# Performance work log

Measured on AMD Instinct MI355X. Metric: run time of the kernel, lower is better.

The kernel has to match this reference:

```python
import jax, jax.numpy as jnp
import numpy as np

D_MODEL = 2048
N_HEADS = 16
HEAD_DIM = D_MODEL // N_HEADS
ROPE_BASE = 10000.0
B, T = 2, 2048


def setup_inputs() -> dict:
    key = jax.random.key(0)
    k1, k2, k3 = jax.random.split(key, 3)
    s_in = 1.0 / np.sqrt(D_MODEL)
    x = jax.random.normal(k1, (B, T, D_MODEL), dtype=jnp.float32)
    Wqkv = jax.random.normal(k2, (3 * D_MODEL, D_MODEL), dtype=jnp.float32) * s_in
    bqkv = jnp.zeros((3 * D_MODEL,), dtype=jnp.float32)
    Wo = jax.random.normal(k3, (D_MODEL, D_MODEL), dtype=jnp.float32) * s_in
    bo = jnp.zeros((D_MODEL,), dtype=jnp.float32)
    return {"x": x, "Wqkv": Wqkv, "bqkv": bqkv, "Wo": Wo, "bo": bo}


def _rotate_half(x):
    # [x1,x2,x3,x4] -> [-x2,x1,-x4,x3] (interleaved pairs)
    x_even = x[..., 0::2]
    x_odd = x[..., 1::2]
    return jnp.stack((-x_odd, x_even), axis=-1).reshape(x.shape)


def _rope_cos_sin(seq_len, dtype):
    half = HEAD_DIM // 2
    inv_freq = 1.0 / (ROPE_BASE ** (jnp.arange(half, dtype=jnp.float32) / half))
    freqs = jnp.arange(seq_len, dtype=jnp.float32)[:, None] * inv_freq[None, :]  # (T, half)
    emb = jnp.repeat(freqs, 2, axis=-1)  # (T, D) interleaved
    cos = jnp.cos(emb).astype(dtype)[None, None]  # (1,1,T,D)
    sin = jnp.sin(emb).astype(dtype)[None, None]
    return cos, sin


def reference(x, Wqkv, bqkv, Wo, bo):
    b, t, c = x.shape
    qkv = jnp.einsum('btc,fc->btf', x, Wqkv) + bqkv  # (B,T,3C)
    q, k, v = jnp.split(qkv, 3, axis=-1)
    def to_heads(z):
        return z.reshape(b, t, N_HEADS, HEAD_DIM).transpose(0, 2, 1, 3)  # (B,H,T,D)
    q, k, v = to_heads(q), to_heads(k), to_heads(v)
    cos, sin = _rope_cos_sin(t, x.dtype)
    q = q * cos + _rotate_half(q) * sin
    k = k * cos + _rotate_half(k) * sin
    scale = 1.0 / jnp.sqrt(jnp.asarray(HEAD_DIM, dtype=x.dtype))
    scores = jnp.einsum('bhqd,bhkd->bhqk', q, k) * scale  # (B,H,T,T)
    causal = jnp.tril(jnp.ones((t, t), dtype=bool))
    scores = jnp.where(causal, scores, jnp.finfo(scores.dtype).min)
    attn = jax.nn.softmax(scores, axis=-1)
    out = jnp.einsum('bhqk,bhkd->bhqd', attn, v)  # (B,H,T,D)
    out = out.transpose(0, 2, 1, 3).reshape(b, t, c)
    return jnp.einsum('btc,oc->bto', out, Wo) + bo
```

## Files before the change

kernel.cpp:

```cpp
#include <hip/hip_runtime.h>

using f16 = _Float16;
typedef _Float16 h8 __attribute__((ext_vector_type(8)));
typedef _Float16 h4 __attribute__((ext_vector_type(4)));
typedef float f4 __attribute__((ext_vector_type(4)));
typedef unsigned int u32;
typedef unsigned long long u64;

#define DEVI static __device__ __forceinline__

DEVI f4 mfma16(h8 a, h8 b, f4 c) {
  return __builtin_amdgcn_mfma_f32_16x16x32_f16(a, b, c, 0, 0, 0);
}

DEVI void gl_lds16(const f16* g, f16* l) {
  __builtin_amdgcn_global_load_lds(
      (const __attribute__((address_space(1))) u32*)g,
      (__attribute__((address_space(3))) u32*)l, 16, 0, 0);
}

DEVI u32 pkh2(float a, float b) {
  union { f16 h[2]; u32 u; } x;
  x.h[0] = (f16)a; x.h[1] = (f16)b;
  return x.u;
}

typedef float fv4 __attribute__((ext_vector_type(4)));

__global__ __launch_bounds__(256) void k_cvt(const float* __restrict__ in,
                                             f16* __restrict__ out, int n4) {
  int i = blockIdx.x * 256 + threadIdx.x;
  if (i >= n4) return;
  fv4 v = ((const fv4*)in)[i];
  h4 o;
  o[0] = (f16)v[0]; o[1] = (f16)v[1]; o[2] = (f16)v[2]; o[3] = (f16)v[3];
  ((h4*)out)[i] = o;
}

__global__ __launch_bounds__(256) void k_rope_tbl(float* __restrict__ tbl) {
  int i = blockIdx.x * 256 + threadIdx.x;
  int t = i >> 6, d = i & 63;
  float invf = exp2f(-(float)d * (13.287712379549449f / 64.f));
  float a = (float)t * invf;
  tbl[2 * i]     = cosf(a);
  tbl[2 * i + 1] = sinf(a);
}

template <int F32OUT>
__global__ __launch_bounds__(512, 2) void k_gemm256(const f16* __restrict__ A,
                                                    const f16* __restrict__ Bt,
                                                    const float* __restrict__ bias,
                                                    void* __restrict__ Cp,
                                                    int M, int N, int K, int gy) {
  __shared__ f16 lds[2][32768];
  const int tid = threadIdx.x;
  const int w = tid >> 6, lane = tid & 63;
  const int g = lane >> 4, colq = lane & 15;
  const int wr = w >> 2, wc = w & 3;
  const int sw = (colq >> 1) & 3;
  const int rdc = (g ^ sw) << 3;

  const int nwg = gridDim.x;
  const int q8 = nwg >> 3;
  const int swz = (blockIdx.x & 7) * q8 + (blockIdx.x >> 3);
  const int bm = swz % gy, bn = swz / gy;

  const f16* Ab = A + (size_t)bm * 256 * K;
  const f16* Bb = Bt + (size_t)bn * 256 * K;
  const int nt = K >> 6;

  const int srow = lane >> 2;
  const int schunk = (lane & 3) ^ ((lane >> 3) & 3);

  auto STAGE_A = [&](int kt, int h, f16* buf) {
    const int k0 = (kt << 6) + (h << 5);
#pragma unroll
    for (int j = 0; j < 2; ++j) {
      const int r = (w * 2 + j) * 16;
      gl_lds16(Ab + (size_t)(r + srow) * K + k0 + schunk * 8, buf + h * 8192 + r * 32);
    }
  };
  auto STAGE_B = [&](int kt, int h, f16* buf) {
    const int k0 = (kt << 6) + (h << 5);
#pragma unroll
    for (int j = 0; j < 2; ++j) {
      const int r = (w * 2 + j) * 16;
      gl_lds16(Bb + (size_t)(r + srow) * K + k0 + schunk * 8, buf + 16384 + h * 8192 + r * 32);
    }
  };

  f4 acc[8][4] = {};

  auto LDA = [&](h8* dst, int mh, int h, const f16* cur) {
#pragma unroll
    for (int m = 0; m < 4; ++m) {
      const int row = wr * 128 + (mh * 4 + m) * 16 + colq;
      dst[m] = *(const h8*)(cur + h * 8192 + row * 32 + rdc);
    }
  };
  auto LDB = [&](h8* dst, int h, const f16* cur) {
#pragma unroll
    for (int n = 0; n < 4; ++n) {
      const int row = wc * 64 + n * 16 + colq;
      dst[n] = *(const h8*)(cur + 16384 + h * 8192 + row * 32 + rdc);
    }
  };
  auto MM = [&](h8* af, h8* bf, int mh) {
#pragma unroll
    for (int m = 0; m < 4; ++m)
#pragma unroll
      for (int n = 0; n < 4; ++n)
        acc[mh * 4 + m][n] = mfma16(af[m], bf[n], acc[mh * 4 + m][n]);
  };

  STAGE_A(0, 0, lds[0]); STAGE_B(0, 0, lds[0]);
  STAGE_A(0, 1, lds[0]); STAGE_B(0, 1, lds[0]);
  STAGE_A(1, 0, lds[1]); STAGE_B(1, 0, lds[1]);
  asm volatile("s_waitcnt vmcnt(4)" ::: "memory");
  __builtin_amdgcn_s_barrier();

  for (int t = 0; t < nt; ++t) {
    f16* cur = lds[t & 1];
    f16* nxt = lds[(t & 1) ^ 1];
    const bool m1 = (t + 1 < nt), m2 = (t + 2 < nt);
    h8 af[4], bf[4];
    LDA(af, 0, 0, cur);
    LDB(bf, 0, cur);
    if (m1) STAGE_A(t + 1, 1, nxt);
    __builtin_amdgcn_s_barrier();
    __builtin_amdgcn_s_setprio(1);
    MM(af, bf, 0);
    __builtin_amdgcn_s_setprio(0);
    __builtin_amdgcn_s_barrier();
    LDA(af, 1, 0, cur);
    if (m1) STAGE_B(t + 1, 1, nxt);
    __builtin_amdgcn_s_barrier();
    __builtin_amdgcn_s_setprio(1);
    MM(af, bf, 1);
    __builtin_amdgcn_s_setprio(0);
    __builtin_amdgcn_s_barrier();
    LDA(af, 0, 1, cur);
    LDB(bf, 1, cur);
    if (m2) STAGE_A(t + 2, 0, cur);
    __builtin_amdgcn_s_barrier();
    __builtin_amdgcn_s_setprio(1);
    MM(af, bf, 0);
    __builtin_amdgcn_s_setprio(0);
    __builtin_amdgcn_s_barrier();
    LDA(af, 1, 1, cur);
    if (m2) STAGE_B(t + 2, 0, cur);
    __builtin_amdgcn_s_barrier();
    __builtin_amdgcn_s_setprio(1);
    MM(af, bf, 1);
    __builtin_amdgcn_s_setprio(0);
    if (m2) {
      asm volatile("s_waitcnt vmcnt(4)" ::: "memory");
    } else {
      asm volatile("s_waitcnt vmcnt(0)" ::: "memory");
    }
    __builtin_amdgcn_s_barrier();
  }

#pragma unroll
  for (int n = 0; n < 4; ++n) {
    const int col = bn * 256 + wc * 64 + n * 16 + colq;
    const float bv = bias[col];
#pragma unroll
    for (int m = 0; m < 8; ++m) {
      const int row0 = bm * 256 + wr * 128 + m * 16 + 4 * g;
#pragma unroll
      for (int r = 0; r < 4; ++r) {
        float v = acc[m][n][r] + bv;
        if constexpr (F32OUT) {
          ((float*)Cp)[(size_t)(row0 + r) * N + col] = v;
        } else {
          ((f16*)Cp)[(size_t)(row0 + r) * N + col] = (f16)v;
        }
      }
    }
  }
}

template <int F32OUT>
__global__ __launch_bounds__(512, 2) void k_gemm128(const f16* __restrict__ A,
                                                    const f16* __restrict__ Bt,
                                                    const float* __restrict__ bias,
                                                    void* __restrict__ Cp,
                                                    int M, int N, int K, int gy) {
  __shared__ f16 lds[2][24576];
  const int tid = threadIdx.x;
  const int w = tid >> 6, lane = tid & 63;
  const int g = lane >> 4, colq = lane & 15;
  const int wr = w >> 2, wc = w & 3;

  const int nwg = gridDim.x;
  const int q8 = nwg >> 3;
  const int swz = (blockIdx.x & 7) * q8 + (blockIdx.x >> 3);
  const int bm = swz % gy, bn = swz / gy;

  const f16* Ab = A + (size_t)bm * 128 * K;
  const f16* Bb = Bt + (size_t)bn * 256 * K;

  const int srow = lane >> 3;
  const int schunk = (lane & 7) ^ srow;
  const int nt = K >> 6;

  auto STAGE = [&](int kt, f16* buf) {
    const int k0 = kt << 6;
    f16* bA = buf;
    f16* bB = buf + 128 * 64;
#pragma unroll
    for (int j = 0; j < 2; ++j) {
      const int r = w * 16 + j * 8;
      gl_lds16(Ab + (size_t)(r + srow) * K + k0 + schunk * 8, bA + r * 64);
    }
#pragma unroll
    for (int j = 0; j < 4; ++j) {
      const int r = w * 32 + j * 8;
      gl_lds16(Bb + (size_t)(r + srow) * K + k0 + schunk * 8, bB + r * 64);
    }
  };

  STAGE(0, lds[0]);
  STAGE(1, lds[1]);
  asm volatile("s_waitcnt vmcnt(6)" ::: "memory");
  __builtin_amdgcn_s_barrier();

  f4 acc[4][4] = {};
  const int rowA0 = wr * 64 + colq;
  const int rowB0 = wc * 64 + colq;
  const int cq7 = colq & 7;

  for (int t = 0; t < nt; ++t) {
    f16* cur = lds[t & 1];
    h8 af[2][4], bf[2][4];
#pragma unroll
    for (int kki = 0; kki < 2; ++kki) {
#pragma unroll
      for (int m = 0; m < 4; ++m)
        af[kki][m] = *(const h8*)(cur + (rowA0 + m * 16) * 64 + (((kki * 4 + g) ^ cq7) * 8));
#pragma unroll
      for (int n = 0; n < 4; ++n)
        bf[kki][n] = *(const h8*)(cur + 8192 + (rowB0 + n * 16) * 64 + (((kki * 4 + g) ^ cq7) * 8));
    }
    asm volatile("s_waitcnt lgkmcnt(0)" ::: "memory");
    __builtin_amdgcn_s_barrier();
    const bool more = (t + 2 < nt);
    if (more) STAGE(t + 2, cur);
    __builtin_amdgcn_s_setprio(1);
#pragma unroll
    for (int m = 0; m < 4; ++m)
#pragma unroll
      for (int n = 0; n < 4; ++n)
#pragma unroll
        for (int kki = 0; kki < 2; ++kki)
          acc[m][n] = mfma16(af[kki][m], bf[kki][n], acc[m][n]);
    __builtin_amdgcn_s_setprio(0);
    if (more) {
      asm volatile("s_waitcnt vmcnt(6)" ::: "memory");
    } else {
      asm volatile("s_waitcnt vmcnt(0)" ::: "memory");
    }
    __builtin_amdgcn_s_barrier();
  }

#pragma unroll
  for (int n = 0; n < 4; ++n) {
    const int col = bn * 256 + wc * 64 + n * 16 + colq;
    const float bv = bias[col];
#pragma unroll
    for (int m = 0; m < 4; ++m) {
      const int row0 = bm * 128 + wr * 64 + m * 16 + 4 * g;
#pragma unroll
      for (int r = 0; r < 4; ++r) {
        float v = acc[m][n][r] + bv;
        if constexpr (F32OUT) {
          ((float*)Cp)[(size_t)(row0 + r) * N + col] = v;
        } else {
          ((f16*)Cp)[(size_t)(row0 + r) * N + col] = (f16)v;
        }
      }
    }
  }
}

__global__ __launch_bounds__(256) void k_rope(const f16* __restrict__ qkv,
                                              const float* __restrict__ tbl,
                                              f16* __restrict__ Q, f16* __restrict__ K) {
  int i = blockIdx.x * 256 + threadIdx.x;
  int d = i & 63;
  int h = (i >> 6) & 15;
  int bt = i >> 10;
  int t = bt & 2047;
  int bh = ((bt >> 11) << 4) | h;
  union { u32 u; f16 h2[2]; } qa, ka, qo, ko;
  qa.u = *(const u32*)(qkv + (size_t)bt * 6144 + h * 128 + 2 * d);
  ka.u = *(const u32*)(qkv + (size_t)bt * 6144 + 2048 + h * 128 + 2 * d);
  float c = tbl[2 * (t * 64 + d)];
  float s = tbl[2 * (t * 64 + d) + 1];
  float q0f = (float)qa.h2[0], q1f = (float)qa.h2[1];
  float k0f = (float)ka.h2[0], k1f = (float)ka.h2[1];
  const float SQ = 0.088388347648318447f * 1.4426950408889634f;
  qo.h2[0] = (f16)((q0f * c - q1f * s) * SQ);
  qo.h2[1] = (f16)((q1f * c + q0f * s) * SQ);
  ko.h2[0] = (f16)(k0f * c - k1f * s);
  ko.h2[1] = (f16)(k1f * c + k0f * s);
  *(u32*)(Q + ((size_t)bh * 2048 + t) * 128 + 2 * d) = qo.u;
  *(u32*)(K + ((size_t)bh * 2048 + t) * 128 + 2 * d) = ko.u;
}

__global__ __launch_bounds__(256) void k_vtrans(const f16* __restrict__ qkv,
                                                f16* __restrict__ Vt) {
  __shared__ f16 ldsT[128 * 40];
  const int bh = blockIdx.y, t0 = blockIdx.x * 32;
  const int b = bh >> 4, h = bh & 15;
  const int tid = threadIdx.x;
#pragma unroll
  for (int cc = 0; cc < 2; ++cc) {
    int task = tid + cc * 256;
    int row = task >> 4;
    int ch = task & 15;
    h8 v = *(const h8*)(qkv + (size_t)(b * 2048 + t0 + row) * 6144 + 4096 + h * 128 + ch * 8);
#pragma unroll
    for (int j = 0; j < 8; ++j) ldsT[(ch * 8 + j) * 40 + row] = v[j];
  }
  __syncthreads();
  int d = tid >> 1, seg = tid & 1;
  h8 v0 = *(const h8*)(ldsT + d * 40 + seg * 16);
  h8 v1 = *(const h8*)(ldsT + d * 40 + seg * 16 + 8);
  f16* dst = Vt + ((size_t)bh * 128 + d) * 2048 + t0 + seg * 16;
  *(h8*)dst = v0;
  *(h8*)(dst + 8) = v1;
}

DEVI void stage_tiles(const f16* __restrict__ Kg, const f16* __restrict__ Vtg,
                      f16* bufK, f16* bufV, int kv, int w, int lane) {
#pragma unroll
  for (int jj = 0; jj < 4; ++jj) {
    const int j = w * 4 + jj;
    const int rK = j * 4 + (lane >> 4);
    const int cK = (lane & 15) ^ ((rK & 7) << 1);
    gl_lds16(Kg + (size_t)(kv + rK) * 128 + cK * 8, bufK + j * 512);
    const int rV = j * 8 + (lane >> 3);
    const int cV = (lane & 7) ^ (rV & 7);
    gl_lds16(Vtg + (size_t)rV * 2048 + kv + cV * 8, bufV + j * 512);
  }
}

__global__ __launch_bounds__(256, 1) void k_attn(const f16* __restrict__ Q,
                                                 const f16* __restrict__ K,
                                                 const f16* __restrict__ Vt,
                                                 f16* __restrict__ O) {
  __shared__ f16 lds[2][16384];
  const int tid = threadIdx.x;
  const int w = tid >> 6, lane = tid & 63;
  const int g = lane >> 4, q = lane & 15;
  const int bid = blockIdx.x;
  const int bh = bid & 31;
  const int b = bid >> 5;

  const f16* Kg = K + (size_t)bh * 2048 * 128;
  const f16* Vtg = Vt + (size_t)bh * 128 * 2048;
  const int qx2 = (q & 7) << 1;
  const int qx = q & 7;

  for (int ph = 0; ph < 2; ++ph) {
    const int p = ph ? (15 - b) : b;
    const int q0w = p * 128 + w * 32;
    const int nit = 2 * (p + 1);

    h8 qf[2][4];
#pragma unroll
    for (int set = 0; set < 2; ++set)
#pragma unroll
      for (int d4 = 0; d4 < 4; ++d4)
        qf[set][d4] = *(const h8*)(Q + ((size_t)bh * 2048 + q0w + 16 * set + q) * 128 + d4 * 32 + g * 8);

    stage_tiles(Kg, Vtg, lds[0], lds[0] + 8192, 0, w, lane);
    asm volatile("s_waitcnt vmcnt(0)" ::: "memory");
    __builtin_amdgcn_s_barrier();

    f4 ot[2][8] = {};
    float mrun[2] = {-3.0e38f, -3.0e38f};
    float lrun[2] = {0.f, 0.f};

    for (int it = 0; it < nit; ++it) {
      const int kv0 = it * 64;
      f16* bufK = lds[it & 1];
      f16* bufV = bufK + 8192;
      if (it + 1 < nit) {
        f16* nb = lds[(it + 1) & 1];
        stage_tiles(Kg, Vtg, nb, nb + 8192, kv0 + 64, w, lane);
      }
      if (kv0 < q0w + 32) {
        f4 st[2][4] = {{{0.f,0.f,0.f,0.f},{0.f,0.f,0.f,0.f},{0.f,0.f,0.f,0.f},{0.f,0.f,0.f,0.f}},
                       {{0.f,0.f,0.f,0.f},{0.f,0.f,0.f,0.f},{0.f,0.f,0.f,0.f},{0.f,0.f,0.f,0.f}}};
#pragma unroll
        for (int d4 = 0; d4 < 4; ++d4) {
          h8 kf[4];
#pragma unroll
          for (int s = 0; s < 4; ++s)
            kf[s] = *(const h8*)(bufK + ((16 * s + q) * 16 + ((4 * d4 + g) ^ qx2)) * 8);
#pragma unroll
          for (int set = 0; set < 2; ++set)
#pragma unroll
            for (int s = 0; s < 4; ++s)
              st[set][s] = mfma16(kf[s], qf[set][d4], st[set][s]);
        }
        if (kv0 + 63 > q0w) {
#pragma unroll
          for (int set = 0; set < 2; ++set) {
            const int qcol = q0w + 16 * set + q;
#pragma unroll
            for (int s = 0; s < 4; ++s)
#pragma unroll
              for (int r = 0; r < 4; ++r)
                if (kv0 + s * 16 + 4 * g + r > qcol) st[set][s][r] = -3.0e38f;
          }
        }
        float pm[2];
#pragma unroll
        for (int set = 0; set < 2; ++set) {
          float m0 = st[set][0][0];
#pragma unroll
          for (int s = 0; s < 4; ++s)
#pragma unroll
            for (int r = 0; r < 4; ++r) m0 = fmaxf(m0, st[set][s][r]);
          m0 = fmaxf(m0, __shfl_xor(m0, 16));
          m0 = fmaxf(m0, __shfl_xor(m0, 32));
          pm[set] = m0;
        }
        const bool ok = (pm[0] <= mrun[0] + 8.0f) && (pm[1] <= mrun[1] + 8.0f);
        if (!__all(ok)) {
#pragma unroll
          for (int set = 0; set < 2; ++set) {
            float mnew = fmaxf(mrun[set], pm[set]);
            float corr = exp2f(mrun[set] - mnew);
            lrun[set] *= corr;
#pragma unroll
            for (int dt = 0; dt < 8; ++dt) ot[set][dt] *= corr;
            mrun[set] = mnew;
          }
        }
#pragma unroll
        for (int set = 0; set < 2; ++set) {
          float ps = 0.f;
#pragma unroll
          for (int s = 0; s < 4; ++s)
#pragma unroll
            for (int r = 0; r < 4; ++r) {
              st[set][s][r] = exp2f(st[set][s][r] - mrun[set]);
              ps += st[set][s][r];
            }
          ps += __shfl_xor(ps, 16);
          ps += __shfl_xor(ps, 32);
          lrun[set] += ps;
        }
        union { u32 u[4]; h8 h; } pb[2][2];
        const int s0l = ((g & 1) << 5) | q;
        const bool hi = g >= 2;
#pragma unroll
        for (int set = 0; set < 2; ++set)
#pragma unroll
          for (int hh = 0; hh < 2; ++hh) {
            u32 wA0 = pkh2(st[set][2 * hh][0], st[set][2 * hh][1]);
            u32 wB0 = pkh2(st[set][2 * hh][2], st[set][2 * hh][3]);
            u32 wA1 = pkh2(st[set][2 * hh + 1][0], st[set][2 * hh + 1][1]);
            u32 wB1 = pkh2(st[set][2 * hh + 1][2], st[set][2 * hh + 1][3]);
            u32 a0 = (u32)__shfl((int)wA0, s0l),      a1 = (u32)__shfl((int)wA1, s0l);
            u32 b0 = (u32)__shfl((int)wB0, s0l),      b1 = (u32)__shfl((int)wB1, s0l);
            u32 c0 = (u32)__shfl((int)wA0, s0l + 16), c1 = (u32)__shfl((int)wA1, s0l + 16);
            u32 d0 = (u32)__shfl((int)wB0, s0l + 16), d1 = (u32)__shfl((int)wB1, s0l + 16);
            pb[set][hh].u[0] = hi ? a1 : a0;
            pb[set][hh].u[1] = hi ? b1 : b0;
            pb[set][hh].u[2] = hi ? c1 : c0;
            pb[set][hh].u[3] = hi ? d1 : d0;
          }
#pragma unroll
        for (int hh = 0; hh < 2; ++hh)
#pragma unroll
          for (int dt = 0; dt < 8; ++dt) {
            h8 vf = *(const h8*)(bufV + ((dt * 16 + q) * 8 + ((4 * hh + g) ^ qx)) * 8);
#pragma unroll
            for (int set = 0; set < 2; ++set)
              ot[set][dt] = mfma16(vf, pb[set][hh].h, ot[set][dt]);
          }
      }
      asm volatile("s_waitcnt vmcnt(0)" ::: "memory");
      __builtin_amdgcn_s_barrier();
    }

#pragma unroll
    for (int set = 0; set < 2; ++set) {
      float linv = 1.0f / lrun[set];
      f16* Ob = O + ((size_t)(bh >> 4) * 2048 + q0w + 16 * set + q) * 2048 + (bh & 15) * 128 + 4 * g;
#pragma unroll
      for (int dt = 0; dt < 8; ++dt) {
        union { f16 hh4[4]; u64 u; } o;
#pragma unroll
        for (int r = 0; r < 4; ++r) o.hh4[r] = (f16)(ot[set][dt][r] * linv);
        *(u64*)(Ob + dt * 16) = o.u;
      }
    }
  }
}

extern "C" void kernel_launch(void* const* d_in, const int* in_sizes, int n_in,
                              void* d_out, int out_size, void* d_ws, size_t ws_size,
                              hipStream_t stream) {
  (void)in_sizes; (void)n_in; (void)out_size; (void)ws_size;
  const float* x    = (const float*)d_in[0];
  const float* Wqkv = (const float*)d_in[1];
  const float* bqkv = (const float*)d_in[2];
  const float* Wo   = (const float*)d_in[3];
  const float* bo   = (const float*)d_in[4];

  char* ws = (char*)d_ws;
  f16* xb    = (f16*)ws; ws += (size_t)4096 * 2048 * 2;
  f16* wqkvb = (f16*)ws; ws += (size_t)6144 * 2048 * 2;
  f16* wob   = (f16*)ws; ws += (size_t)2048 * 2048 * 2;
  f16* qkvb  = (f16*)ws; ws += (size_t)4096 * 6144 * 2;
  f16* Qb    = (f16*)ws; ws += (size_t)32 * 2048 * 128 * 2;
  f16* Kb    = (f16*)ws; ws += (size_t)32 * 2048 * 128 * 2;
  f16* Vtb   = (f16*)ws; ws += (size_t)32 * 128 * 2048 * 2;
  f16* attb  = (f16*)ws; ws += (size_t)4096 * 2048 * 2;
  float* tbl = (float*)ws; ws += (size_t)2048 * 64 * 2 * 4;

  k_cvt<<<8192, 256, 0, stream>>>(x, xb, 2097152);
  k_cvt<<<12288, 256, 0, stream>>>(Wqkv, wqkvb, 3145728);
  k_cvt<<<4096, 256, 0, stream>>>(Wo, wob, 1048576);
  k_rope_tbl<<<512, 256, 0, stream>>>(tbl);

  k_gemm256<0><<<384, 512, 0, stream>>>(xb, wqkvb, bqkv, qkvb, 4096, 6144, 2048, 16);

  k_rope<<<16384, 256, 0, stream>>>(qkvb, tbl, Qb, Kb);
  k_vtrans<<<dim3(64, 32), 256, 0, stream>>>(qkvb, Vtb);

  k_attn<<<256, 256, 0, stream>>>(Qb, Kb, Vtb, attb);

  k_gemm128<1><<<256, 512, 0, stream>>>(attb, wob, bo, d_out, 4096, 2048, 2048, 32);
}
```

Before: 326.2 us.

## Double-buffer GEMM register fragments and fuse RoPE with V transpose kernel

The QKV GEMM main loop now keeps two sets of A/B fragments, so the LDS reads for the next MFMA quarter are issued before the current MFMAs, and half of the barriers are removed. Launch bounds drop from two to one workgroup per CU to make room for the extra registers. Separately, the RoPE kernel is merged into the V-transpose kernel, which removes one launch and lets the Q/K rotation share a pass over each tile. Removing barriers risks LDS races with the staging writes, and the lower occupancy could reduce latency hiding.

```diff
diff --git a/kernel.cpp b/kernel.cpp
--- a/kernel.cpp
+++ b/kernel.cpp
@@ -47,7 +47,7 @@
 }
 
 template <int F32OUT>
-__global__ __launch_bounds__(512, 2) void k_gemm256(const f16* __restrict__ A,
+__global__ __launch_bounds__(512, 1) void k_gemm256(const f16* __restrict__ A,
                                                     const f16* __restrict__ Bt,
                                                     const float* __restrict__ bias,
                                                     void* __restrict__ Cp,
@@ -119,39 +119,36 @@
   asm volatile("s_waitcnt vmcnt(4)" ::: "memory");
   __builtin_amdgcn_s_barrier();
 
+  h8 af0[4], af1[4], bf0[4], bf1[4];
+
   for (int t = 0; t < nt; ++t) {
     f16* cur = lds[t & 1];
     f16* nxt = lds[(t & 1) ^ 1];
     const bool m1 = (t + 1 < nt), m2 = (t + 2 < nt);
-    h8 af[4], bf[4];
-    LDA(af, 0, 0, cur);
-    LDB(bf, 0, cur);
+    LDA(af0, 0, 0, cur);
+    LDB(bf0, 0, cur);
     if (m1) STAGE_A(t + 1, 1, nxt);
-    __builtin_amdgcn_s_barrier();
+    LDA(af1, 1, 0, cur);
     __builtin_amdgcn_s_setprio(1);
-    MM(af, bf, 0);
+    MM(af0, bf0, 0);
     __builtin_amdgcn_s_setprio(0);
     __builtin_amdgcn_s_barrier();
-    LDA(af, 1, 0, cur);
     if (m1) STAGE_B(t + 1, 1, nxt);
-    __builtin_amdgcn_s_barrier();
+    LDA(af0, 0, 1, cur);
+    LDB(bf1, 1, cur);
     __builtin_amdgcn_s_setprio(1);
-    MM(af, bf, 1);
+    MM(af1, bf0, 1);
     __builtin_amdgcn_s_setprio(0);
     __builtin_amdgcn_s_barrier();
-    LDA(af, 0, 1, cur);
-    LDB(bf, 1, cur);
     if (m2) STAGE_A(t + 2, 0, cur);
-    __builtin_amdgcn_s_barrier();
+    LDA(af1, 1, 1, cur);
     __builtin_amdgcn_s_setprio(1);
-    MM(af, bf, 0);
+    MM(af0, bf1, 0);
     __builtin_amdgcn_s_setprio(0);
     __builtin_amdgcn_s_barrier();
-    LDA(af, 1, 1, cur);
     if (m2) STAGE_B(t + 2, 0, cur);
-    __builtin_amdgcn_s_barrier();
     __builtin_amdgcn_s_setprio(1);
-    MM(af, bf, 1);
+    MM(af1, bf1, 1);
     __builtin_amdgcn_s_setprio(0);
     if (m2) {
       asm volatile("s_waitcnt vmcnt(4)" ::: "memory");
@@ -284,33 +281,10 @@
   }
 }
 
-__global__ __launch_bounds__(256) void k_rope(const f16* __restrict__ qkv,
-                                              const float* __restrict__ tbl,
-                                              f16* __restrict__ Q, f16* __restrict__ K) {
-  int i = blockIdx.x * 256 + threadIdx.x;
-  int d = i & 63;
-  int h = (i >> 6) & 15;
-  int bt = i >> 10;
-  int t = bt & 2047;
-  int bh = ((bt >> 11) << 4) | h;
-  union { u32 u; f16 h2[2]; } qa, ka, qo, ko;
-  qa.u = *(const u32*)(qkv + (size_t)bt * 6144 + h * 128 + 2 * d);
-  ka.u = *(const u32*)(qkv + (size_t)bt * 6144 + 2048 + h * 128 + 2 * d);
-  float c = tbl[2 * (t * 64 + d)];
-  float s = tbl[2 * (t * 64 + d) + 1];
-  float q0f = (float)qa.h2[0], q1f = (float)qa.h2[1];
-  float k0f = (float)ka.h2[0], k1f = (float)ka.h2[1];
-  const float SQ = 0.088388347648318447f * 1.4426950408889634f;
-  qo.h2[0] = (f16)((q0f * c - q1f * s) * SQ);
-  qo.h2[1] = (f16)((q1f * c + q0f * s) * SQ);
-  ko.h2[0] = (f16)(k0f * c - k1f * s);
-  ko.h2[1] = (f16)(k1f * c + k0f * s);
-  *(u32*)(Q + ((size_t)bh * 2048 + t) * 128 + 2 * d) = qo.u;
-  *(u32*)(K + ((size_t)bh * 2048 + t) * 128 + 2 * d) = ko.u;
-}
-
-__global__ __launch_bounds__(256) void k_vtrans(const f16* __restrict__ qkv,
-                                                f16* __restrict__ Vt) {
+__global__ __launch_bounds__(256) void k_ropev(const f16* __restrict__ qkv,
+                                               const float* __restrict__ tbl,
+                                               f16* __restrict__ Q, f16* __restrict__ K,
+                                               f16* __restrict__ Vt) {
   __shared__ f16 ldsT[128 * 40];
   const int bh = blockIdx.y, t0 = blockIdx.x * 32;
   const int b = bh >> 4, h = bh & 15;
@@ -323,6 +297,28 @@
     h8 v = *(const h8*)(qkv + (size_t)(b * 2048 + t0 + row) * 6144 + 4096 + h * 128 + ch * 8);
 #pragma unroll
     for (int j = 0; j < 8; ++j) ldsT[(ch * 8 + j) * 40 + row] = v[j];
+  }
+  const float SQ = 0.088388347648318447f * 1.4426950408889634f;
+#pragma unroll
+  for (int cc = 0; cc < 8; ++cc) {
+    int task = tid + cc * 256;
+    int row = task >> 6;
+    int d = task & 63;
+    int t = t0 + row;
+    const f16* src = qkv + (size_t)(b * 2048 + t) * 6144 + h * 128 + 2 * d;
+    union { u32 u; f16 h2[2]; } qa, ka, qo, ko;
+    qa.u = *(const u32*)src;
+    ka.u = *(const u32*)(src + 2048);
+    float c = tbl[2 * (t * 64 + d)];
+    float s = tbl[2 * (t * 64 + d) + 1];
+    float q0f = (float)qa.h2[0], q1f = (float)qa.h2[1];
+    float k0f = (float)ka.h2[0], k1f = (float)ka.h2[1];
+    qo.h2[0] = (f16)((q0f * c - q1f * s) * SQ);
+    qo.h2[1] = (f16)((q1f * c + q0f * s) * SQ);
+    ko.h2[0] = (f16)(k0f * c - k1f * s);
+    ko.h2[1] = (f16)(k1f * c + k0f * s);
+    *(u32*)(Q + ((size_t)bh * 2048 + t) * 128 + 2 * d) = qo.u;
+    *(u32*)(K + ((size_t)bh * 2048 + t) * 128 + 2 * d) = ko.u;
   }
   __syncthreads();
   int d = tid >> 1, seg = tid & 1;
@@ -533,8 +529,7 @@
 
   k_gemm256<0><<<384, 512, 0, stream>>>(xb, wqkvb, bqkv, qkvb, 4096, 6144, 2048, 16);
 
-  k_rope<<<16384, 256, 0, stream>>>(qkvb, tbl, Qb, Kb);
-  k_vtrans<<<dim3(64, 32), 256, 0, stream>>>(qkvb, Vtb);
+  k_ropev<<<dim3(64, 32), 256, 0, stream>>>(qkvb, tbl, Qb, Kb, Vtb);
 
   k_attn<<<256, 256, 0, stream>>>(Qb, Kb, Vtb, attb);
 
```

Result: no change. 321.0 us (-1.6%).
